# Kernel optimization log

Hardware: AMD Instinct MI355X
Metric: run time of the kernel (lower is better)

The kernel has to match this reference:

```python
import jax, jax.numpy as jnp
import numpy as np

QLEN, BSZ, D_MODEL = 1024, 4, 1024
N_HEAD, D_HEAD = 16, 64
NEG = -1e30


def _layer_norm(x, g, b, eps=1e-5):
    mu = jnp.mean(x, axis=-1, keepdims=True)
    var = jnp.mean((x - mu) ** 2, axis=-1, keepdims=True)
    return (x - mu) / jnp.sqrt(var + eps) * g + b


def _rel_shift(x):
    # x: [qlen, klen, bsz, n_head] -- Transformer-XL relative shift
    q, k, b, n = x.shape
    x = jnp.pad(x, ((0, 0), (1, 0), (0, 0), (0, 0)))  # zero-pad along klen front
    x = x.reshape(k + 1, q, b, n)[1:]
    return x.reshape(q, k, b, n)


def setup_inputs() -> dict:
    key = jax.random.key(0)
    ks = jax.random.split(key, 8)
    s = 0.02
    w = jax.random.normal(ks[0], (QLEN, BSZ, D_MODEL), jnp.float32)
    r = jax.random.normal(ks[1], (QLEN, D_MODEL), jnp.float32)
    r_w_bias = jax.random.normal(ks[2], (N_HEAD, D_HEAD), jnp.float32) * s
    r_r_bias = jax.random.normal(ks[3], (N_HEAD, D_HEAD), jnp.float32) * s
    attn_mask = jnp.tril(jnp.ones((QLEN, QLEN), dtype=bool))  # causal: True = attend
    W_qkv = jax.random.normal(ks[4], (D_MODEL, 3 * N_HEAD * D_HEAD), jnp.float32) * s
    W_r = jax.random.normal(ks[5], (D_MODEL, N_HEAD * D_HEAD), jnp.float32) * s
    W_o = jax.random.normal(ks[6], (N_HEAD * D_HEAD, D_MODEL), jnp.float32) * s
    gamma = jnp.ones((D_MODEL,), jnp.float32)
    beta = jnp.zeros((D_MODEL,), jnp.float32)
    return {"w": w, "r": r, "r_w_bias": r_w_bias, "r_r_bias": r_r_bias,
            "attn_mask": attn_mask, "W_qkv": W_qkv, "W_r": W_r, "W_o": W_o,
            "gamma": gamma, "beta": beta}


def reference(w, r, r_w_bias, r_r_bias, attn_mask, W_qkv, W_r, W_o, gamma, beta):
    qlen, bsz, _ = w.shape
    scale = 1.0 / (D_HEAD ** 0.5)
    heads = w @ W_qkv                                    # [q, b, 3*n*d]
    q_h, k_h, v_h = jnp.split(heads, 3, axis=-1)
    q_h = q_h.reshape(qlen, bsz, N_HEAD, D_HEAD)
    k_h = k_h.reshape(qlen, bsz, N_HEAD, D_HEAD)
    v_h = v_h.reshape(qlen, bsz, N_HEAD, D_HEAD)
    r_k = (r @ W_r).reshape(-1, N_HEAD, D_HEAD)          # [rlen, n, d]
    AC = jnp.einsum('ibnd,jbnd->ijbn', q_h + r_w_bias, k_h)
    BD = jnp.einsum('ibnd,jnd->ijbn', q_h + r_r_bias, r_k)
    BD = _rel_shift(BD)
    score = (AC + BD) * scale                            # [q, k, b, n]
    score = jnp.where(attn_mask[:, :, None, None], score, NEG)
    prob = jax.nn.softmax(score, axis=1)
    vec = jnp.einsum('ijbn,jbnd->ibnd', prob, v_h).reshape(qlen, bsz, N_HEAD * D_HEAD)
    attn_out = vec @ W_o
    return _layer_norm(w + attn_out, gamma, beta)
```

## Files before the change

kernel.cpp:

```cpp
#include <hip/hip_runtime.h>
#include <math.h>

constexpr int QLEN_C  = 1024;
constexpr int BSZ_C   = 4;
constexpr int DMODEL  = 1024;
constexpr float SCALE = 0.125f;
constexpr float NEGF  = -1e30f;

typedef __attribute__((ext_vector_type(8))) short bh8;
typedef __attribute__((ext_vector_type(4))) float f32x4;

__device__ inline short f2bf(float f) {
    union { float f; unsigned u; } v; v.f = f;
    unsigned r = v.u + 0x7FFFu + ((v.u >> 16) & 1u);
    return (short)(r >> 16);
}
__device__ inline float bf2f(short s) {
    union { unsigned u; float f; } v;
    v.u = ((unsigned)(unsigned short)s) << 16;
    return v.f;
}
__device__ inline void gload16(const void* g, void* l) {
    __builtin_amdgcn_global_load_lds(
        (__attribute__((address_space(1))) void*)g,
        (__attribute__((address_space(3))) void*)l, 16, 0, 0);
}
__device__ inline void wave_lds_fence() {
    __builtin_amdgcn_sched_barrier(0);
    __builtin_amdgcn_s_waitcnt(0xC07F);
    __builtin_amdgcn_sched_barrier(0);
}
__device__ inline void block_sync() {
    __builtin_amdgcn_sched_barrier(0);
    __builtin_amdgcn_s_barrier();
    __builtin_amdgcn_sched_barrier(0);
}
__device__ inline void wait_vm8() {
    __builtin_amdgcn_sched_barrier(0);
    asm volatile("s_waitcnt vmcnt(8)" ::: "memory");
    __builtin_amdgcn_sched_barrier(0);
}
__device__ inline void wait_vm0() {
    __builtin_amdgcn_sched_barrier(0);
    asm volatile("s_waitcnt vmcnt(0)" ::: "memory");
    __builtin_amdgcn_sched_barrier(0);
}

__global__ __launch_bounds__(512, 2)
void gemm12_8ph(const short* __restrict__ wb, const short* __restrict__ WqkvT,
                short* __restrict__ headsb,
                const short* __restrict__ rb, const short* __restrict__ WrT,
                short* __restrict__ rkb)
{
    constexpr int NT = 16;
    __shared__ alignas(16) short Ald[2][2][128][64];
    __shared__ alignas(16) short Bld[2][2][128][64];

    const int bid0 = blockIdx.x;
    const int bid = (bid0 & 7) * 26 + (bid0 >> 3);

    const short* A; const short* BT; short* Cc; int Nn; int bx, by;
    if (bid < 192) {
        A = wb; BT = WqkvT; Cc = headsb; Nn = 3072;
        bx = bid % 12; by = bid / 12;
    } else {
        int q = bid - 192;
        A = rb; BT = WrT; Cc = rkb; Nn = 1024;
        bx = q & 3; by = q >> 2;
    }
    const int row0 = by * 256, col0 = bx * 256;

    const int tid = threadIdx.x;
    const int wid = tid >> 6, lane = tid & 63;
    const int quad = lane >> 4, c = lane & 15;
    const int wr = wid >> 2, wcn = wid & 3;
    const int hb = wcn >> 1;

    auto stage_half = [&](short* dst, const short* src, int srcRow0, int kcol) {
        const int r0 = tid >> 3, b0 = tid & 7;
        gload16(src + (size_t)(srcRow0 + r0) * 1024 + kcol + ((b0 ^ (r0 & 7)) * 8),
                (char*)dst + tid * 16);
        const int t2 = tid + 512;
        const int r1 = t2 >> 3, b1 = t2 & 7;
        gload16(src + (size_t)(srcRow0 + r1) * 1024 + kcol + ((b1 ^ (r1 & 7)) * 8),
                (char*)dst + t2 * 16);
    };

    f32x4 acc[8][4];
    #pragma unroll
    for (int mf = 0; mf < 8; ++mf)
        #pragma unroll
        for (int nf = 0; nf < 4; ++nf) acc[mf][nf] = (f32x4)0.0f;

    stage_half(&Ald[0][0][0][0], A, row0,        0);
    stage_half(&Ald[0][1][0][0], A, row0 + 128,  0);
    stage_half(&Bld[0][0][0][0], BT, col0,       0);
    stage_half(&Bld[0][1][0][0], BT, col0 + 128, 0);
    stage_half(&Ald[1][0][0][0], A, row0,        64);
    stage_half(&Ald[1][1][0][0], A, row0 + 128,  64);
    stage_half(&Bld[1][0][0][0], BT, col0,       64);
    stage_half(&Bld[1][1][0][0], BT, col0 + 128, 64);
    wait_vm8();
    block_sync();

    for (int t = 0; t < NT; ++t) {
        const int d = t & 1;

        bh8 aF[8][2], bF[4][2];
        #pragma unroll
        for (int mf = 0; mf < 8; ++mf)
            #pragma unroll
            for (int ks = 0; ks < 2; ++ks)
                aF[mf][ks] = *(const bh8*)&Ald[d][wr][mf * 16 + c]
                                 [((ks * 4 + quad) ^ (c & 7)) * 8];
        #pragma unroll
        for (int nf = 0; nf < 4; ++nf)
            #pragma unroll
            for (int ks = 0; ks < 2; ++ks)
                bF[nf][ks] = *(const bh8*)&Bld[d][hb][(wcn & 1) * 64 + nf * 16 + c]
                                 [((ks * 4 + quad) ^ (c & 7)) * 8];

        wave_lds_fence();
        block_sync();

        const int ts = t + 2;

        __builtin_amdgcn_s_setprio(1);
        #pragma unroll
        for (int mf = 0; mf < 4; ++mf)
            #pragma unroll
            for (int nf = 0; nf < 2; ++nf) {
                acc[mf][nf] = __builtin_amdgcn_mfma_f32_16x16x32_bf16(aF[mf][0], bF[nf][0], acc[mf][nf], 0, 0, 0);
                acc[mf][nf] = __builtin_amdgcn_mfma_f32_16x16x32_bf16(aF[mf][1], bF[nf][1], acc[mf][nf], 0, 0, 0);
            }
        __builtin_amdgcn_s_setprio(0);

        if (ts < NT) {
            stage_half(&Ald[d][0][0][0], A, row0,       ts * 64);
            stage_half(&Ald[d][1][0][0], A, row0 + 128, ts * 64);
        }

        __builtin_amdgcn_s_setprio(1);
        #pragma unroll
        for (int mf = 0; mf < 4; ++mf)
            #pragma unroll
            for (int nf = 2; nf < 4; ++nf) {
                acc[mf][nf] = __builtin_amdgcn_mfma_f32_16x16x32_bf16(aF[mf][0], bF[nf][0], acc[mf][nf], 0, 0, 0);
                acc[mf][nf] = __builtin_amdgcn_mfma_f32_16x16x32_bf16(aF[mf][1], bF[nf][1], acc[mf][nf], 0, 0, 0);
            }
        __builtin_amdgcn_s_setprio(0);

        if (ts < NT) {
            stage_half(&Bld[d][0][0][0], BT, col0,       ts * 64);
            stage_half(&Bld[d][1][0][0], BT, col0 + 128, ts * 64);
        }

        __builtin_amdgcn_s_setprio(1);
        #pragma unroll
        for (int mf = 4; mf < 8; ++mf)
            #pragma unroll
            for (int nf = 0; nf < 2; ++nf) {
                acc[mf][nf] = __builtin_amdgcn_mfma_f32_16x16x32_bf16(aF[mf][0], bF[nf][0], acc[mf][nf], 0, 0, 0);
                acc[mf][nf] = __builtin_amdgcn_mfma_f32_16x16x32_bf16(aF[mf][1], bF[nf][1], acc[mf][nf], 0, 0, 0);
            }
        #pragma unroll
        for (int mf = 4; mf < 8; ++mf)
            #pragma unroll
            for (int nf = 2; nf < 4; ++nf) {
                acc[mf][nf] = __builtin_amdgcn_mfma_f32_16x16x32_bf16(aF[mf][0], bF[nf][0], acc[mf][nf], 0, 0, 0);
                acc[mf][nf] = __builtin_amdgcn_mfma_f32_16x16x32_bf16(aF[mf][1], bF[nf][1], acc[mf][nf], 0, 0, 0);
            }
        __builtin_amdgcn_s_setprio(0);

        if (t + 2 < NT)      wait_vm8();
        else if (t + 1 < NT) wait_vm0();
        if (t + 1 < NT)      block_sync();
    }

    wave_lds_fence();
    block_sync();
    short* cst = &Ald[0][0][0][0];
    const int crow = tid >> 2, cseg = tid & 3;
    #pragma unroll
    for (int pass = 0; pass < 2; ++pass) {
        if (wr == pass) {
            #pragma unroll
            for (int mf = 0; mf < 8; ++mf)
                #pragma unroll
                for (int nf = 0; nf < 4; ++nf)
                    #pragma unroll
                    for (int rr = 0; rr < 4; ++rr)
                        cst[(mf * 16 + quad * 4 + rr) * 256 + wcn * 64 + nf * 16 + c] =
                            f2bf(acc[mf][nf][rr]);
        }
        wave_lds_fence();
        block_sync();
        {
            short* gp = Cc + (size_t)(row0 + pass * 128 + crow) * Nn + col0 + cseg * 64;
            const short* lp = &cst[crow * 256 + cseg * 64];
            #pragma unroll
            for (int u = 0; u < 8; ++u)
                *(bh8*)(gp + u * 8) = *(const bh8*)(lp + u * 8);
        }
        if (pass == 0) { wave_lds_fence(); block_sync(); }
    }
}

__global__ __launch_bounds__(256)
void gemm_wo_sk(const short* __restrict__ A, const short* __restrict__ BT,
                float* __restrict__ C0, float* __restrict__ C1)
{
    constexpr int BK = 32;
    constexpr int N  = 1024, K = 1024;
    __shared__ alignas(16) short As[128 * BK];
    __shared__ alignas(16) short Bs[128 * BK];

    const int bid0 = blockIdx.x;
    const int bid = (bid0 & 7) * 64 + (bid0 >> 3);
    const int half = bid & 1, tile = bid >> 1;
    const int bx = tile & 7, by = tile >> 3;
    const int k_lo = half * 512;
    float* C = half ? C1 : C0;

    const int tid = threadIdx.x;
    const int wave = tid >> 6, lane = tid & 63;
    const int quad = lane >> 4, c = lane & 15;
    const int wr = wave >> 1, wc = wave & 1;
    const int row0 = by * 128, col0 = bx * 128;

    const int ch0 = wave * 128 + lane, ch1 = ch0 + 64;
    const int m0 = ch0 >> 2, s0 = ch0 & 3;
    const int m1 = ch1 >> 2, s1 = ch1 & 3;

    f32x4 acc[4][4];
    #pragma unroll
    for (int i = 0; i < 4; ++i)
        #pragma unroll
        for (int j = 0; j < 4; ++j) acc[i][j] = (f32x4)0.0f;

    for (int k0 = k_lo; k0 < k_lo + 512; k0 += BK) {
        gload16(A  + (size_t)(row0 + m0) * K + k0 + s0 * 8, (char*)As + ch0 * 16);
        gload16(A  + (size_t)(row0 + m1) * K + k0 + s1 * 8, (char*)As + ch1 * 16);
        gload16(BT + (size_t)(col0 + m0) * K + k0 + s0 * 8, (char*)Bs + ch0 * 16);
        gload16(BT + (size_t)(col0 + m1) * K + k0 + s1 * 8, (char*)Bs + ch1 * 16);
        __syncthreads();

        bh8 aF[4], bF[4];
        #pragma unroll
        for (int mi = 0; mi < 4; ++mi)
            aF[mi] = *(const bh8*)&As[(wr * 64 + mi * 16 + c) * BK + quad * 8];
        #pragma unroll
        for (int ni = 0; ni < 4; ++ni)
            bF[ni] = *(const bh8*)&Bs[(wc * 64 + ni * 16 + c) * BK + quad * 8];
        #pragma unroll
        for (int mi = 0; mi < 4; ++mi)
            #pragma unroll
            for (int ni = 0; ni < 4; ++ni)
                acc[mi][ni] = __builtin_amdgcn_mfma_f32_16x16x32_bf16(
                    aF[mi], bF[ni], acc[mi][ni], 0, 0, 0);
        __syncthreads();
    }

    #pragma unroll
    for (int mi = 0; mi < 4; ++mi)
        #pragma unroll
        for (int ni = 0; ni < 4; ++ni)
            #pragma unroll
            for (int r = 0; r < 4; ++r) {
                int orow = row0 + wr * 64 + mi * 16 + quad * 4 + r;
                int ocol = col0 + wc * 64 + ni * 16 + c;
                C[(size_t)orow * N + ocol] = acc[mi][ni][r];
            }
}

__device__ inline void transp_tile(const float* __restrict__ B, short* __restrict__ BT,
                                   int K, int N, int n0, int k0, int t,
                                   float (*tile)[68])
{
    const int row = t >> 2, c4 = t & 3;
    const float* src = B + (size_t)(k0 + row) * N + n0 + c4 * 16;
    #pragma unroll
    for (int u = 0; u < 4; ++u) {
        float4 v = *(const float4*)(src + u * 4);
        tile[row][c4 * 16 + u * 4 + 0] = v.x;
        tile[row][c4 * 16 + u * 4 + 1] = v.y;
        tile[row][c4 * 16 + u * 4 + 2] = v.z;
        tile[row][c4 * 16 + u * 4 + 3] = v.w;
    }
    __syncthreads();
    const int nl = t >> 2, kc = t & 3;
    short tmp[16];
    #pragma unroll
    for (int e = 0; e < 16; ++e) tmp[e] = f2bf(tile[kc * 16 + e][nl]);
    short* dst = BT + (size_t)(n0 + nl) * K + k0 + kc * 16;
    *(bh8*)dst = *(bh8*)&tmp[0];
    *(bh8*)(dst + 8) = *(bh8*)&tmp[8];
}

__global__ __launch_bounds__(256)
void prep_all(const float* __restrict__ w, const float* __restrict__ r,
              const float* __restrict__ Wqkv, const float* __restrict__ Wr,
              const float* __restrict__ Wo,
              short* __restrict__ wb, short* __restrict__ rb,
              short* __restrict__ WqkvT, short* __restrict__ WrT,
              short* __restrict__ WoT, short* __restrict__ rkb)
{
    __shared__ float tile[64][68];
    const int bid = blockIdx.x;
    const int t = threadIdx.x;

    if (bid < 2048) {
        int idx = (bid * 256 + t) * 8;
        bh8 o;
        #pragma unroll
        for (int e = 0; e < 8; ++e) o[e] = f2bf(w[idx + e]);
        *(bh8*)(wb + idx) = o;
    } else if (bid < 2560) {
        int idx = ((bid - 2048) * 256 + t) * 8;
        bh8 o;
        #pragma unroll
        for (int e = 0; e < 8; ++e) o[e] = f2bf(r[idx + e]);
        *(bh8*)(rb + idx) = o;
    } else if (bid < 3328) {
        int tt = bid - 2560;
        transp_tile(Wqkv, WqkvT, 1024, 3072, (tt % 48) * 64, (tt / 48) * 64, t, tile);
    } else if (bid < 3584) {
        int tt = bid - 3328;
        transp_tile(Wr, WrT, 1024, 1024, (tt % 16) * 64, (tt / 16) * 64, t, tile);
    } else if (bid < 3840) {
        int tt = bid - 3584;
        transp_tile(Wo, WoT, 1024, 1024, (tt % 16) * 64, (tt / 16) * 64, t, tile);
    } else {
        int idx = 1024 * 1024 + ((bid - 3840) * 256 + t) * 8;
        bh8 z;
        #pragma unroll
        for (int e = 0; e < 8; ++e) z[e] = 0;
        *(bh8*)(rkb + idx) = z;
    }
}

__global__ __launch_bounds__(256)
void prep_kv2(const short* __restrict__ headsb, const short* __restrict__ rkb,
              short* __restrict__ kfrag, short* __restrict__ vfrag,
              short* __restrict__ rfrag)
{
    __shared__ short vtile[64][72];
    const int blk = blockIdx.x;
    const int t = threadIdx.x;

    if (blk < 1024) {
        const int bn = blk >> 4, ju = blk & 15;
        const int b = bn & 3, nn = bn >> 2;
        const int j0 = ju * 64;
        const int row = t >> 2, d0 = (t & 3) * 16;

        const short* kp = headsb + ((size_t)(j0 + row) * 4 + b) * 3072 + 1024 + nn * 64 + d0;
        const short* vp = kp + 1024;
        bh8 k0 = *(const bh8*)kp, k1 = *(const bh8*)(kp + 8);
        bh8 v0 = *(const bh8*)vp, v1 = *(const bh8*)(vp + 8);

        {
            const int jtile = (j0 + row) >> 4, cc = row & 15;
            short* kb_bn = kfrag + (size_t)bn * 65536 + (size_t)jtile * 1024 + cc * 8;
            const int d1 = d0 + 8;
            *(bh8*)(kb_bn + (d0 >> 5) * 512 + ((d0 >> 3) & 3) * 128) = k0;
            *(bh8*)(kb_bn + (d1 >> 5) * 512 + ((d1 >> 3) & 3) * 128) = k1;
        }
        #pragma unroll
        for (int e = 0; e < 8; ++e) {
            vtile[row][d0 + e] = v0[e];
            vtile[row][d0 + 8 + e] = v1[e];
        }
        __syncthreads();
        const int d = t >> 2, jl0 = (t & 3) * 16;
        short tmp[16];
        #pragma unroll
        for (int e = 0; e < 16; ++e) tmp[e] = vtile[jl0 + e][d];
        short* vb = vfrag + (size_t)bn * 65536 + (size_t)ju * 4096
                  + (d >> 4) * 1024 + (d & 15) * 8;
        const int jl1 = jl0 + 8;
        *(bh8*)(vb + (jl0 >> 5) * 512 + ((jl0 >> 3) & 3) * 128) = *(bh8*)&tmp[0];
        *(bh8*)(vb + (jl1 >> 5) * 512 + ((jl1 >> 3) & 3) * 128) = *(bh8*)&tmp[8];
    } else {
        const int rblk = blk - 1024;
        const int row = rblk * 4 + (t >> 6);
        const int col0 = (t & 63) * 16;
        const short* src = rkb + (size_t)row * 1024 + col0;
        bh8 r0 = *(const bh8*)src, r1 = *(const bh8*)(src + 8);
        const int rt = row >> 4, cc = row & 15;
        const int nn = col0 >> 6, dd = col0 & 63, dd1 = dd + 8;
        short* dst = rfrag + (size_t)rt * 16384 + nn * 1024 + cc * 8;
        *(bh8*)(dst + (dd  >> 5) * 512 + ((dd  >> 3) & 3) * 128) = r0;
        *(bh8*)(dst + (dd1 >> 5) * 512 + ((dd1 >> 3) & 3) * 128) = r1;
    }
}

__global__ __launch_bounds__(256)
void attn_mfma(const short* __restrict__ headsb, const short* __restrict__ rfrag,
               const short* __restrict__ kfrag, const short* __restrict__ vfrag,
               const float* __restrict__ rwb, const float* __restrict__ rrb,
               short* __restrict__ vecb)
{
    __shared__ alignas(16) short sP[4][2][16 * 80];

    const int tid = threadIdx.x;
    const int wave = tid >> 6, lane = tid & 63;
    const int quad = lane >> 4, c = lane & 15;

    const int bi = blockIdx.x;
    const int itile = 15 - (bi >> 6);
    const int bn = bi & 63;
    const int n = bn >> 2, b = bn & 3;
    const int nU = itile + 1;
    const int rb = itile * 64 + wave * 16;

    const int dq = n * 64 + quad * 8;
    const short* kbp = kfrag + (size_t)bn * 65536;
    const short* vtp = vfrag + (size_t)bn * 65536;
    const int lin = quad * 128 + c * 8;

    bh8 ones;
    #pragma unroll
    for (int e = 0; e < 8; ++e) ones[e] = (short)0x3F80;

    bh8 aAC[2], aBD[2];
    #pragma unroll
    for (int ks = 0; ks < 2; ++ks) {
        const short* qp = headsb + ((size_t)(rb + c) * 4 + b) * 3072 + dq + 32 * ks;
        bh8 q8 = *(const bh8*)qp;
        #pragma unroll
        for (int e = 0; e < 8; ++e) {
            float qv = bf2f(q8[e]);
            aAC[ks][e] = f2bf(qv + rwb[dq + 32 * ks + e]);
            aBD[ks][e] = f2bf(qv + rrb[dq + 32 * ks + e]);
        }
    }

    bh8 rkv[10], kbv[8];
    auto pf = [&](int j0) {
        const int rt0 = (1008 - rb + j0) >> 4;
        #pragma unroll
        for (int tt = 0; tt < 5; ++tt) {
            const short* rp = rfrag + (size_t)(rt0 + tt) * 16384 + n * 1024 + lin;
            rkv[2 * tt]     = *(const bh8*)rp;
            rkv[2 * tt + 1] = *(const bh8*)(rp + 512);
        }
        const int jt0 = j0 >> 4;
        #pragma unroll
        for (int jt = 0; jt < 4; ++jt) {
            const short* kp = kbp + (size_t)(jt0 + jt) * 1024 + lin;
            kbv[2 * jt]     = *(const bh8*)kp;
            kbv[2 * jt + 1] = *(const bh8*)(kp + 512);
        }
    };

    f32x4 oacc[4], lacc;
    #pragma unroll
    for (int dt = 0; dt < 4; ++dt) oacc[dt] = (f32x4)0.0f;
    lacc = (f32x4)0.0f;

    pf(0);
    int j0 = 0;

    for (int u = 0; u < nU; ++u) {
        short* PL = &sP[wave][u & 1][0];

        bh8 vvv[8];
        {
            const short* vup = vtp + (size_t)(j0 >> 6) * 4096;
            #pragma unroll
            for (int dt = 0; dt < 4; ++dt) {
                const short* vp = vup + dt * 1024 + lin;
                vvv[2 * dt]     = *(const bh8*)vp;
                vvv[2 * dt + 1] = *(const bh8*)(vp + 512);
            }
        }

        f32x4 bt[5];
        #pragma unroll
        for (int tt = 0; tt < 5; ++tt) {
            bt[tt] = (f32x4)0.0f;
            bt[tt] = __builtin_amdgcn_mfma_f32_16x16x32_bf16(aBD[0], rkv[2 * tt], bt[tt], 0, 0, 0);
            bt[tt] = __builtin_amdgcn_mfma_f32_16x16x32_bf16(aBD[1], rkv[2 * tt + 1], bt[tt], 0, 0, 0);
        }
        f32x4 ac[4];
        #pragma unroll
        for (int jt = 0; jt < 4; ++jt) {
            ac[jt] = (f32x4)0.0f;
            ac[jt] = __builtin_amdgcn_mfma_f32_16x16x32_bf16(aAC[0], kbv[2 * jt], ac[jt], 0, 0, 0);
            ac[jt] = __builtin_amdgcn_mfma_f32_16x16x32_bf16(aAC[1], kbv[2 * jt + 1], ac[jt], 0, 0, 0);
        }

        if (u + 1 < nU) pf(j0 + 64);

        #pragma unroll
        for (int r = 0; r < 4; ++r) {
            const int row = quad * 4 + r;
            const int o = 15 - row;
            const int src = (lane & 48) | ((c + o) & 15);
            const int gi = rb + row;
            #pragma unroll
            for (int jt = 0; jt < 4; ++jt) {
                float sval = (c < o) ? bt[jt + 1][r] : bt[jt][r];
                float bd = __shfl(sval, src, 64);
                int gj = j0 + c + 16 * jt;
                float v = SCALE * (ac[jt][r] + bd);
                PL[row * 80 + c + 16 * jt] = (gj > gi) ? (short)0 : f2bf(__expf(v));
            }
        }

        wave_lds_fence();

        bh8 aP[2];
        #pragma unroll
        for (int ks = 0; ks < 2; ++ks)
            aP[ks] = *(const bh8*)(PL + c * 80 + 32 * ks + quad * 8);
        #pragma unroll
        for (int dt = 0; dt < 4; ++dt) {
            oacc[dt] = __builtin_amdgcn_mfma_f32_16x16x32_bf16(aP[0], vvv[2 * dt], oacc[dt], 0, 0, 0);
            oacc[dt] = __builtin_amdgcn_mfma_f32_16x16x32_bf16(aP[1], vvv[2 * dt + 1], oacc[dt], 0, 0, 0);
        }
        lacc = __builtin_amdgcn_mfma_f32_16x16x32_bf16(aP[0], ones, lacc, 0, 0, 0);
        lacc = __builtin_amdgcn_mfma_f32_16x16x32_bf16(aP[1], ones, lacc, 0, 0, 0);

        j0 += 64;
    }

    #pragma unroll
    for (int r = 0; r < 4; ++r) {
        float rinv = 1.f / lacc[r];
        int gi = rb + quad * 4 + r;
        short* op = vecb + ((size_t)gi * 4 + b) * 1024 + n * 64;
        #pragma unroll
        for (int dt = 0; dt < 4; ++dt)
            op[c + 16 * dt] = f2bf(oacc[dt][r] * rinv);
    }
}

__global__ __launch_bounds__(256)
void ln_kernel(const float* __restrict__ w, const float* __restrict__ a0,
               const float* __restrict__ a1,
               const float* __restrict__ gamma, const float* __restrict__ beta,
               float* __restrict__ out)
{
    const int row = blockIdx.x;
    const int tid = threadIdx.x;
    const float4* xw4 = (const float4*)(w  + (size_t)row * DMODEL);
    const float4* p04 = (const float4*)(a0 + (size_t)row * DMODEL);
    const float4* p14 = (const float4*)(a1 + (size_t)row * DMODEL);

    float4 a = xw4[tid], b0 = p04[tid], b1 = p14[tid];
    float x[4] = {a.x + b0.x + b1.x, a.y + b0.y + b1.y,
                  a.z + b0.z + b1.z, a.w + b0.w + b1.w};
    float s = x[0] + x[1] + x[2] + x[3];

    __shared__ float red[6];
    #pragma unroll
    for (int m = 1; m < 64; m <<= 1) s += __shfl_xor(s, m, 64);
    int wv = tid >> 6, lnid = tid & 63;
    if (lnid == 0) red[wv] = s;
    __syncthreads();
    if (tid == 0) red[4] = red[0] + red[1] + red[2] + red[3];
    __syncthreads();
    float mu = red[4] * (1.f / DMODEL);

    float vs = 0.f;
    #pragma unroll
    for (int e = 0; e < 4; ++e) { float d = x[e] - mu; vs += d * d; }
    #pragma unroll
    for (int m = 1; m < 64; m <<= 1) vs += __shfl_xor(vs, m, 64);
    if (lnid == 0) red[wv] = vs;
    __syncthreads();
    if (tid == 0) red[5] = red[0] + red[1] + red[2] + red[3];
    __syncthreads();
    float var = red[5] * (1.f / DMODEL);
    float inv = rsqrtf(var + 1e-5f);

    float4 g = ((const float4*)gamma)[tid];
    float4 be = ((const float4*)beta)[tid];
    float4 o;
    o.x = (x[0] - mu) * inv * g.x + be.x;
    o.y = (x[1] - mu) * inv * g.y + be.y;
    o.z = (x[2] - mu) * inv * g.z + be.z;
    o.w = (x[3] - mu) * inv * g.w + be.w;
    ((float4*)(out + (size_t)row * DMODEL))[tid] = o;
}

extern "C" void kernel_launch(void* const* d_in, const int* in_sizes, int n_in,
                              void* d_out, int out_size, void* d_ws, size_t ws_size,
                              hipStream_t stream)
{
    const float* w     = (const float*)d_in[0];
    const float* r     = (const float*)d_in[1];
    const float* rwb   = (const float*)d_in[2];
    const float* rrb   = (const float*)d_in[3];
    const float* Wqkv  = (const float*)d_in[5];
    const float* Wr    = (const float*)d_in[6];
    const float* Wo    = (const float*)d_in[7];
    const float* gamma = (const float*)d_in[8];
    const float* beta  = (const float*)d_in[9];
    float* out = (float*)d_out;

    short* headsb = (short*)d_ws;
    short* wb     = headsb + 12582912;
    short* WqkvT  = wb + 4194304;
    short* rb     = WqkvT + 3145728;
    short* WrT    = rb + 1048576;
    short* WoT    = WrT + 1048576;
    short* rkb    = WoT + 1048576;
    short* kfrag  = rkb + 1114112;
    short* vfrag  = kfrag + 4194304;
    short* vecb   = vfrag + 4194304;

    short* rfrag  = rb;

    float* attno0 = (float*)headsb;
    float* attno1 = (float*)wb;

    prep_all<<<3872, 256, 0, stream>>>(w, r, Wqkv, Wr, Wo, wb, rb, WqkvT, WrT, WoT, rkb);
    gemm12_8ph<<<dim3(208), 512, 0, stream>>>(wb, WqkvT, headsb, rb, WrT, rkb);
    prep_kv2<<<dim3(1296), 256, 0, stream>>>(headsb, rkb, kfrag, vfrag, rfrag);
    attn_mfma<<<dim3(1024), 256, 0, stream>>>(headsb, rfrag, kfrag, vfrag, rwb, rrb, vecb);
    gemm_wo_sk<<<dim3(512), 256, 0, stream>>>(vecb, WoT, attno0, attno1);
    ln_kernel<<<4096, 256, 0, stream>>>(w, attno0, attno1, gamma, beta, out);
}
```

Baseline: 129.4 us.

## Rewrite Wo GEMM as double-buffered 256x128 tile kernel with interleaved loads

Replaces the simple single-buffered split-K Wo GEMM (128x128 tiles, BK=32, two syncthreads per step) with a 512-thread kernel using 256x128 tiles, BK=64, double-buffered LDS with XOR swizzle, and global-to-LDS loads interleaved between MFMA groups under raised wave priority. The goal is to hide global load latency behind MFMA work, cut LDS bank conflicts, and raise data reuse per tile. The cost is a larger LDS footprint, more registers per thread, and half as many blocks (256), which may underfill the CUs.

```diff
diff --git a/kernel.cpp b/kernel.cpp
--- a/kernel.cpp
+++ b/kernel.cpp
@@ -38,6 +38,11 @@
 __device__ inline void wait_vm8() {
     __builtin_amdgcn_sched_barrier(0);
     asm volatile("s_waitcnt vmcnt(8)" ::: "memory");
+    __builtin_amdgcn_sched_barrier(0);
+}
+__device__ inline void wait_vm6() {
+    __builtin_amdgcn_sched_barrier(0);
+    asm volatile("s_waitcnt vmcnt(6)" ::: "memory");
     __builtin_amdgcn_sched_barrier(0);
 }
 __device__ inline void wait_vm0() {
@@ -206,70 +211,127 @@
     }
 }
 
-__global__ __launch_bounds__(256)
-void gemm_wo_sk(const short* __restrict__ A, const short* __restrict__ BT,
-                float* __restrict__ C0, float* __restrict__ C1)
-{
-    constexpr int BK = 32;
-    constexpr int N  = 1024, K = 1024;
-    __shared__ alignas(16) short As[128 * BK];
-    __shared__ alignas(16) short Bs[128 * BK];
+__global__ __launch_bounds__(512, 2)
+void gemm_wo_8ph(const short* __restrict__ A, const short* __restrict__ BT,
+                 float* __restrict__ C0, float* __restrict__ C1)
+{
+    constexpr int NT = 8;
+    constexpr int N  = 1024;
+    __shared__ alignas(16) short Ald[2][2][128][64];
+    __shared__ alignas(16) short Bld[2][128][64];
 
     const int bid0 = blockIdx.x;
-    const int bid = (bid0 & 7) * 64 + (bid0 >> 3);
+    const int bid = (bid0 & 7) * 32 + (bid0 >> 3);
     const int half = bid & 1, tile = bid >> 1;
-    const int bx = tile & 7, by = tile >> 3;
+    const int by = tile >> 3, bx = tile & 7;
+    const int row0 = by * 256, col0 = bx * 128;
     const int k_lo = half * 512;
     float* C = half ? C1 : C0;
 
     const int tid = threadIdx.x;
-    const int wave = tid >> 6, lane = tid & 63;
+    const int wid = tid >> 6, lane = tid & 63;
     const int quad = lane >> 4, c = lane & 15;
-    const int wr = wave >> 1, wc = wave & 1;
-    const int row0 = by * 128, col0 = bx * 128;
-
-    const int ch0 = wave * 128 + lane, ch1 = ch0 + 64;
-    const int m0 = ch0 >> 2, s0 = ch0 & 3;
-    const int m1 = ch1 >> 2, s1 = ch1 & 3;
-
-    f32x4 acc[4][4];
-    #pragma unroll
-    for (int i = 0; i < 4; ++i)
-        #pragma unroll
-        for (int j = 0; j < 4; ++j) acc[i][j] = (f32x4)0.0f;
-
-    for (int k0 = k_lo; k0 < k_lo + 512; k0 += BK) {
-        gload16(A  + (size_t)(row0 + m0) * K + k0 + s0 * 8, (char*)As + ch0 * 16);
-        gload16(A  + (size_t)(row0 + m1) * K + k0 + s1 * 8, (char*)As + ch1 * 16);
-        gload16(BT + (size_t)(col0 + m0) * K + k0 + s0 * 8, (char*)Bs + ch0 * 16);
-        gload16(BT + (size_t)(col0 + m1) * K + k0 + s1 * 8, (char*)Bs + ch1 * 16);
-        __syncthreads();
-
-        bh8 aF[4], bF[4];
-        #pragma unroll
-        for (int mi = 0; mi < 4; ++mi)
-            aF[mi] = *(const bh8*)&As[(wr * 64 + mi * 16 + c) * BK + quad * 8];
-        #pragma unroll
-        for (int ni = 0; ni < 4; ++ni)
-            bF[ni] = *(const bh8*)&Bs[(wc * 64 + ni * 16 + c) * BK + quad * 8];
-        #pragma unroll
-        for (int mi = 0; mi < 4; ++mi)
-            #pragma unroll
-            for (int ni = 0; ni < 4; ++ni)
-                acc[mi][ni] = __builtin_amdgcn_mfma_f32_16x16x32_bf16(
-                    aF[mi], bF[ni], acc[mi][ni], 0, 0, 0);
-        __syncthreads();
-    }
-
-    #pragma unroll
-    for (int mi = 0; mi < 4; ++mi)
-        #pragma unroll
-        for (int ni = 0; ni < 4; ++ni)
-            #pragma unroll
-            for (int r = 0; r < 4; ++r) {
-                int orow = row0 + wr * 64 + mi * 16 + quad * 4 + r;
-                int ocol = col0 + wc * 64 + ni * 16 + c;
-                C[(size_t)orow * N + ocol] = acc[mi][ni][r];
+    const int wr = wid >> 2, wcn = wid & 3;
+
+    auto stage_half = [&](short* dst, const short* src, int srcRow0, int kcol) {
+        const int r0 = tid >> 3, b0 = tid & 7;
+        gload16(src + (size_t)(srcRow0 + r0) * 1024 + kcol + ((b0 ^ (r0 & 7)) * 8),
+                (char*)dst + tid * 16);
+        const int t2 = tid + 512;
+        const int r1 = t2 >> 3, b1 = t2 & 7;
+        gload16(src + (size_t)(srcRow0 + r1) * 1024 + kcol + ((b1 ^ (r1 & 7)) * 8),
+                (char*)dst + t2 * 16);
+    };
+
+    f32x4 acc[8][2];
+    #pragma unroll
+    for (int mf = 0; mf < 8; ++mf)
+        #pragma unroll
+        for (int nf = 0; nf < 2; ++nf) acc[mf][nf] = (f32x4)0.0f;
+
+    stage_half(&Ald[0][0][0][0], A, row0,        k_lo);
+    stage_half(&Ald[0][1][0][0], A, row0 + 128,  k_lo);
+    stage_half(&Bld[0][0][0],    BT, col0,       k_lo);
+    stage_half(&Ald[1][0][0][0], A, row0,        k_lo + 64);
+    stage_half(&Ald[1][1][0][0], A, row0 + 128,  k_lo + 64);
+    stage_half(&Bld[1][0][0],    BT, col0,       k_lo + 64);
+    wait_vm6();
+    block_sync();
+
+    for (int t = 0; t < NT; ++t) {
+        const int d = t & 1;
+
+        bh8 aF[8][2], bF[2][2];
+        #pragma unroll
+        for (int mf = 0; mf < 8; ++mf)
+            #pragma unroll
+            for (int ks = 0; ks < 2; ++ks)
+                aF[mf][ks] = *(const bh8*)&Ald[d][wr][mf * 16 + c]
+                                 [((ks * 4 + quad) ^ (c & 7)) * 8];
+        #pragma unroll
+        for (int nf = 0; nf < 2; ++nf)
+            #pragma unroll
+            for (int ks = 0; ks < 2; ++ks)
+                bF[nf][ks] = *(const bh8*)&Bld[d][wcn * 32 + nf * 16 + c]
+                                 [((ks * 4 + quad) ^ (c & 7)) * 8];
+
+        wave_lds_fence();
+        block_sync();
+
+        const int ts = t + 2;
+        const int kc = k_lo + ts * 64;
+
+        __builtin_amdgcn_s_setprio(1);
+        #pragma unroll
+        for (int mf = 0; mf < 4; ++mf)
+            #pragma unroll
+            for (int nf = 0; nf < 2; ++nf) {
+                acc[mf][nf] = __builtin_amdgcn_mfma_f32_16x16x32_bf16(aF[mf][0], bF[nf][0], acc[mf][nf], 0, 0, 0);
+                acc[mf][nf] = __builtin_amdgcn_mfma_f32_16x16x32_bf16(aF[mf][1], bF[nf][1], acc[mf][nf], 0, 0, 0);
+            }
+        __builtin_amdgcn_s_setprio(0);
+
+        if (ts < NT) {
+            stage_half(&Ald[d][0][0][0], A, row0,       kc);
+            stage_half(&Ald[d][1][0][0], A, row0 + 128, kc);
+        }
+
+        __builtin_amdgcn_s_setprio(1);
+        #pragma unroll
+        for (int mf = 4; mf < 6; ++mf)
+            #pragma unroll
+            for (int nf = 0; nf < 2; ++nf) {
+                acc[mf][nf] = __builtin_amdgcn_mfma_f32_16x16x32_bf16(aF[mf][0], bF[nf][0], acc[mf][nf], 0, 0, 0);
+                acc[mf][nf] = __builtin_amdgcn_mfma_f32_16x16x32_bf16(aF[mf][1], bF[nf][1], acc[mf][nf], 0, 0, 0);
+            }
+        __builtin_amdgcn_s_setprio(0);
+
+        if (ts < NT) stage_half(&Bld[d][0][0], BT, col0, kc);
+
+        __builtin_amdgcn_s_setprio(1);
+        #pragma unroll
+        for (int mf = 6; mf < 8; ++mf)
+            #pragma unroll
+            for (int nf = 0; nf < 2; ++nf) {
+                acc[mf][nf] = __builtin_amdgcn_mfma_f32_16x16x32_bf16(aF[mf][0], bF[nf][0], acc[mf][nf], 0, 0, 0);
+                acc[mf][nf] = __builtin_amdgcn_mfma_f32_16x16x32_bf16(aF[mf][1], bF[nf][1], acc[mf][nf], 0, 0, 0);
+            }
+        __builtin_amdgcn_s_setprio(0);
+
+        if (t + 2 < NT)      wait_vm6();
+        else if (t + 1 < NT) wait_vm0();
+        if (t + 1 < NT)      block_sync();
+    }
+
+    #pragma unroll
+    for (int mf = 0; mf < 8; ++mf)
+        #pragma unroll
+        for (int nf = 0; nf < 2; ++nf)
+            #pragma unroll
+            for (int rr = 0; rr < 4; ++rr) {
+                int orow = row0 + wr * 128 + mf * 16 + quad * 4 + rr;
+                int ocol = col0 + wcn * 32 + nf * 16 + c;
+                C[(size_t)orow * N + ocol] = acc[mf][nf][rr];
             }
 }
 
@@ -621,6 +683,6 @@
     gemm12_8ph<<<dim3(208), 512, 0, stream>>>(wb, WqkvT, headsb, rb, WrT, rkb);
     prep_kv2<<<dim3(1296), 256, 0, stream>>>(headsb, rkb, kfrag, vfrag, rfrag);
     attn_mfma<<<dim3(1024), 256, 0, stream>>>(headsb, rfrag, kfrag, vfrag, rwb, rrb, vecb);
-    gemm_wo_sk<<<dim3(512), 256, 0, stream>>>(vecb, WoT, attno0, attno1);
+    gemm_wo_8ph<<<dim3(256), 512, 0, stream>>>(vecb, WoT, attno0, attno1);
     ln_kernel<<<4096, 256, 0, stream>>>(w, attno0, attno1, gamma, beta, out);
 }
```

New measurement: 127.6 us. About the same (-1.4%).
